# Optimization experiments

Hardware: AMD Instinct MI355X
Metric: run time of the kernel (lower is better)

The kernel has to match this reference:

```python
import jax, jax.numpy as jnp
import numpy as np

B, T, C = 4, 2048, 768
NH = 12
HD = C // NH  # 64


def setup_inputs() -> dict:
    key = jax.random.key(0)
    k1, k2, k3 = jax.random.split(key, 3)
    x = jax.random.normal(k1, (B, T, C), dtype=jnp.float32)
    W_attn = jax.random.normal(k2, (C, 3 * C), dtype=jnp.float32) * (1.0 / np.sqrt(C))
    b_attn = jnp.zeros((3 * C,), dtype=jnp.float32)
    W_proj = jax.random.normal(k3, (C, C), dtype=jnp.float32) * (1.0 / np.sqrt(C))
    b_proj = jnp.zeros((C,), dtype=jnp.float32)
    return {"x": x, "W_attn": W_attn, "b_attn": b_attn, "W_proj": W_proj, "b_proj": b_proj}


def reference(x, W_attn, b_attn, W_proj, b_proj):
    b, t, c = x.shape
    nh, hd = NH, c // NH
    qkv = x @ W_attn + b_attn                      # (B,T,3C)
    q, k, v = jnp.split(qkv, 3, axis=2)
    # (B,T,C) -> (B,NH,T,HD)
    q = q.reshape(b, t, nh, hd).transpose(0, 2, 1, 3)
    k = k.reshape(b, t, nh, hd).transpose(0, 2, 1, 3)
    v = v.reshape(b, t, nh, hd).transpose(0, 2, 1, 3)
    att = jnp.einsum('bhqd,bhkd->bhqk', q, k) / jnp.sqrt(jnp.float32(hd))
    causal = jnp.tril(jnp.ones((t, t), dtype=bool))
    att = jnp.where(causal, att, -jnp.inf)
    att = jax.nn.softmax(att, axis=-1)
    y = jnp.einsum('bhqk,bhkd->bhqd', att, v)      # (B,NH,T,HD)
    y = y.transpose(0, 2, 1, 3).reshape(b, t, c)
    return y @ W_proj + b_proj
```

## Files before the change

### kernel.cpp

```cpp
#include <hip/hip_runtime.h>
#include <hip/hip_bf16.h>
#include <cstdint>

typedef __bf16 bf16;
typedef __bf16 bf16x4 __attribute__((ext_vector_type(4)));
typedef __bf16 bf16x8 __attribute__((ext_vector_type(8)));
typedef float f32x4 __attribute__((ext_vector_type(4)));

#define B_  4
#define T_  2048
#define C_  768
#define NH_ 12
#define HD_ 64
#define BH_ (B_ * NH_)

__device__ __forceinline__ f32x4 mfma16(bf16x8 a, bf16x8 b, f32x4 c) {
  return __builtin_amdgcn_mfma_f32_16x16x32_bf16(a, b, c, 0, 0, 0);
}

__device__ __forceinline__ void gload16(const bf16* src, bf16* dst) {
  __builtin_amdgcn_global_load_lds(
      (const __attribute__((address_space(1))) unsigned int*)src,
      (__attribute__((address_space(3))) unsigned int*)dst, 16, 0, 0);
}

__global__ __launch_bounds__(256) void cvt_kernel(const float* __restrict__ in,
                                                  bf16* __restrict__ out, int n4) {
  int i = blockIdx.x * blockDim.x + threadIdx.x;
  if (i < n4) {
    float4 v = reinterpret_cast<const float4*>(in)[i];
    bf16x4 o;
    o[0] = (bf16)v.x; o[1] = (bf16)v.y; o[2] = (bf16)v.z; o[3] = (bf16)v.w;
    reinterpret_cast<bf16x4*>(out)[i] = o;
  }
}

__global__ __launch_bounds__(256) void wtr_kernel(const float* __restrict__ W,
                                                  bf16* __restrict__ WT, int K, int N) {
  __shared__ bf16 t[64][72];
  const int tid = threadIdx.x;
  const int k0 = blockIdx.x * 64, n0 = blockIdx.y * 64;
  {
    const int r = tid >> 2, cg = (tid & 3) * 16;
    const float* src = W + (size_t)(k0 + r) * N + n0 + cg;
    float4 a0 = reinterpret_cast<const float4*>(src)[0];
    float4 a1 = reinterpret_cast<const float4*>(src)[1];
    float4 a2 = reinterpret_cast<const float4*>(src)[2];
    float4 a3 = reinterpret_cast<const float4*>(src)[3];
    bf16x8 lo, hi;
    lo[0]=(bf16)a0.x; lo[1]=(bf16)a0.y; lo[2]=(bf16)a0.z; lo[3]=(bf16)a0.w;
    lo[4]=(bf16)a1.x; lo[5]=(bf16)a1.y; lo[6]=(bf16)a1.z; lo[7]=(bf16)a1.w;
    hi[0]=(bf16)a2.x; hi[1]=(bf16)a2.y; hi[2]=(bf16)a2.z; hi[3]=(bf16)a2.w;
    hi[4]=(bf16)a3.x; hi[5]=(bf16)a3.y; hi[6]=(bf16)a3.z; hi[7]=(bf16)a3.w;
    *reinterpret_cast<bf16x8*>(&t[r][cg]) = lo;
    *reinterpret_cast<bf16x8*>(&t[r][cg + 8]) = hi;
  }
  __syncthreads();
  {
    const int n = tid & 63, kg = (tid >> 6) * 16;
    bf16x8 o0, o1;
#pragma unroll
    for (int i = 0; i < 8; ++i) { o0[i] = t[kg + i][n]; o1[i] = t[kg + 8 + i][n]; }
    bf16* dst = WT + (size_t)(n0 + n) * K + k0 + kg;
    *reinterpret_cast<bf16x8*>(dst) = o0;
    *reinterpret_cast<bf16x8*>(dst + 8) = o1;
  }
}

template <int EPI>
__global__ __launch_bounds__(256) void gemm_mfma(
    const bf16* __restrict__ A, const bf16* __restrict__ BT,
    const float* __restrict__ bias, int M, int N, int K,
    bf16* __restrict__ q, bf16* __restrict__ k_, bf16* __restrict__ v,
    float* __restrict__ out) {
  __shared__ bf16 AlF[128 * 32];
  __shared__ bf16 BlF[128 * 32];

  const int tid = threadIdx.x;
  const int wid = tid >> 6, lane = tid & 63;
  const int m0 = blockIdx.y * 128, n0 = blockIdx.x * 128;
  const int wm = (wid >> 1) * 64, wn = (wid & 1) * 64;
  const int r = lane & 15, g = lane >> 4;

  f32x4 acc[4][4] = {};

  const int srow = tid >> 2;
  const int scol = (tid & 3) * 8;

  for (int k0 = 0; k0 < K; k0 += 32) {
    __syncthreads();
#pragma unroll
    for (int c = 0; c < 2; ++c) {
      gload16(A  + (size_t)(m0 + c * 64 + srow) * K + k0 + scol, AlF + c * 2048 + wid * 512);
      gload16(BT + (size_t)(n0 + c * 64 + srow) * K + k0 + scol, BlF + c * 2048 + wid * 512);
    }
    __syncthreads();

    bf16x8 af[4], bfr[4];
#pragma unroll
    for (int fm = 0; fm < 4; ++fm)
      af[fm] = *reinterpret_cast<bf16x8*>(&AlF[(wm + fm * 16 + r) * 32 + g * 8]);
#pragma unroll
    for (int fn = 0; fn < 4; ++fn)
      bfr[fn] = *reinterpret_cast<bf16x8*>(&BlF[(wn + fn * 16 + r) * 32 + g * 8]);
#pragma unroll
    for (int fm = 0; fm < 4; ++fm)
#pragma unroll
      for (int fn = 0; fn < 4; ++fn)
        acc[fm][fn] = mfma16(af[fm], bfr[fn], acc[fm][fn]);
  }

#pragma unroll
  for (int fm = 0; fm < 4; ++fm)
#pragma unroll
    for (int fn = 0; fn < 4; ++fn)
#pragma unroll
      for (int j = 0; j < 4; ++j) {
        int m = m0 + wm + fm * 16 + g * 4 + j;
        int n = n0 + wn + fn * 16 + r;
        float val = acc[fm][fn][j] + bias[n];
        if (EPI == 0) {
          int b = m >> 11, t = m & 2047;
          bf16* dst; int c;
          if (n < 768)        { dst = q;  c = n;        val *= 0.125f; }
          else if (n < 1536)  { dst = k_; c = n - 768;  }
          else                { dst = v;  c = n - 1536; }
          int h = c >> 6, d = c & 63;
          dst[(((size_t)(b * NH_ + h)) * T_ + t) * HD_ + d] = (bf16)val;
        } else {
          out[(size_t)m * N + n] = val;
        }
      }
}

__global__ __launch_bounds__(256) void attn_fwd(
    const bf16* __restrict__ Q, const bf16* __restrict__ K,
    const bf16* __restrict__ V, bf16* __restrict__ Y) {
  __shared__ bf16 Kl[64][72];
  __shared__ bf16 VtF[64 * 72];
  __shared__ bf16 Pl[4][16][72];

  const int tid = threadIdx.x;
  const int wid = tid >> 6, lane = tid & 63;
  const int r = lane & 15, g = lane >> 4;
  const int bh = blockIdx.y;
  const int bidx = bh / NH_, h = bh % NH_;

  const bf16* Qb = Q + (size_t)bh * T_ * HD_;
  const bf16* Kb = K + (size_t)bh * T_ * HD_;
  const bf16* Vb = V + (size_t)bh * T_ * HD_;

  const int krow = tid >> 3;
  const int kc8 = (tid & 7) * 8;

#pragma unroll
  for (int pass = 0; pass < 2; ++pass) {
    const int tile = pass ? 31 - blockIdx.x : blockIdx.x;
    const int qt0 = tile * 64 + wid * 16;

    bf16x8 qf[2];
#pragma unroll
    for (int kc = 0; kc < 2; ++kc)
      qf[kc] = *reinterpret_cast<const bf16x8*>(
          Qb + (size_t)(qt0 + r) * HD_ + kc * 32 + g * 8);

    float m_st[4], l_st[4];
    f32x4 o[4] = {};
#pragma unroll
    for (int j = 0; j < 4; ++j) { m_st[j] = -INFINITY; l_st[j] = 0.f; }

    const int nsteps = tile + 1;
    for (int s = 0; s < nsteps; ++s) {
      const int kv0 = s * 64;
      __syncthreads();
#pragma unroll
      for (int p = 0; p < 2; ++p) {
        int row = p * 32 + krow;
        bf16x8 kv8 = *reinterpret_cast<const bf16x8*>(Kb + (size_t)(kv0 + row) * HD_ + kc8);
        *reinterpret_cast<bf16x8*>(&Kl[row][kc8]) = kv8;
        bf16x8 vv8 = *reinterpret_cast<const bf16x8*>(Vb + (size_t)(kv0 + row) * HD_ + kc8);
        int xorb = (((row >> 3) ^ (tid & 7)) << 3) + (row & 7);
#pragma unroll
        for (int j = 0; j < 8; ++j) VtF[(kc8 + j) * 72 + xorb] = vv8[j];
      }
      __syncthreads();

      f32x4 s4[4] = {};
      __builtin_amdgcn_s_setprio(1);
#pragma unroll
      for (int cb = 0; cb < 4; ++cb)
#pragma unroll
        for (int kc = 0; kc < 2; ++kc) {
          bf16x8 kf = *reinterpret_cast<bf16x8*>(&Kl[cb * 16 + r][kc * 32 + g * 8]);
          s4[cb] = mfma16(qf[kc], kf, s4[cb]);
        }
      __builtin_amdgcn_s_setprio(0);

      if (kv0 + 63 > qt0) {
#pragma unroll
        for (int cb = 0; cb < 4; ++cb)
#pragma unroll
          for (int j = 0; j < 4; ++j) {
            int qr = qt0 + g * 4 + j;
            int kc_ = kv0 + cb * 16 + r;
            if (kc_ > qr) s4[cb][j] = -INFINITY;
          }
      }

      float p[4][4];
#pragma unroll
      for (int j = 0; j < 4; ++j) {
        float mm = fmaxf(fmaxf(s4[0][j], s4[1][j]), fmaxf(s4[2][j], s4[3][j]));
#pragma unroll
        for (int msk = 1; msk < 16; msk <<= 1) mm = fmaxf(mm, __shfl_xor(mm, msk));
        float mn = fmaxf(m_st[j], mm);
        float sc = __expf(m_st[j] - mn);
        float sum = 0.f;
#pragma unroll
        for (int cb = 0; cb < 4; ++cb) {
          float pv = __expf(s4[cb][j] - mn);
          p[cb][j] = pv;
          sum += pv;
        }
#pragma unroll
        for (int msk = 1; msk < 16; msk <<= 1) sum += __shfl_xor(sum, msk);
        l_st[j] = l_st[j] * sc + sum;
        m_st[j] = mn;
#pragma unroll
        for (int dn = 0; dn < 4; ++dn) o[dn][j] *= sc;
      }

#pragma unroll
      for (int cb = 0; cb < 4; ++cb)
#pragma unroll
        for (int j = 0; j < 4; ++j)
          Pl[wid][g * 4 + j][cb * 16 + r] = (bf16)p[cb][j];

      __builtin_amdgcn_s_setprio(1);
#pragma unroll
      for (int kc = 0; kc < 2; ++kc) {
        bf16x8 pf = *reinterpret_cast<bf16x8*>(&Pl[wid][r][kc * 32 + g * 8]);
#pragma unroll
        for (int dn = 0; dn < 4; ++dn) {
          int d = dn * 16 + r;
          bf16x8 vf = *reinterpret_cast<bf16x8*>(
              &VtF[d * 72 + (((4 * kc + g) ^ (d >> 3)) << 3)]);
          o[dn] = mfma16(pf, vf, o[dn]);
        }
      }
      __builtin_amdgcn_s_setprio(0);
    }

#pragma unroll
    for (int j = 0; j < 4; ++j) {
      float inv = 1.f / l_st[j];
      int qrow = qt0 + g * 4 + j;
#pragma unroll
      for (int dn = 0; dn < 4; ++dn) {
        int d = dn * 16 + r;
        Y[((size_t)bidx * T_ + qrow) * C_ + h * HD_ + d] = (bf16)(o[dn][j] * inv);
      }
    }
  }
}

extern "C" void kernel_launch(void* const* d_in, const int* in_sizes, int n_in,
                              void* d_out, int out_size, void* d_ws, size_t ws_size,
                              hipStream_t stream) {
  const float* x  = (const float*)d_in[0];
  const float* Wa = (const float*)d_in[1];
  const float* ba = (const float*)d_in[2];
  const float* Wp = (const float*)d_in[3];
  const float* bp = (const float*)d_in[4];
  float* out = (float*)d_out;

  char* ws = (char*)d_ws;
  size_t off = 0;
  auto alloc = [&](size_t bytes) {
    char* p = ws + off;
    off += (bytes + 255) & ~(size_t)255;
    return p;
  };
  bf16* xb   = (bf16*)alloc((size_t)B_ * T_ * C_ * 2);
  bf16* WaT  = (bf16*)alloc((size_t)C_ * 3 * C_ * 2);
  bf16* WpT  = (bf16*)alloc((size_t)C_ * C_ * 2);
  bf16* Qb   = (bf16*)alloc((size_t)BH_ * T_ * HD_ * 2);
  bf16* Kb   = (bf16*)alloc((size_t)BH_ * T_ * HD_ * 2);
  bf16* Vb   = (bf16*)alloc((size_t)BH_ * T_ * HD_ * 2);
  bf16* Yb   = (bf16*)alloc((size_t)B_ * T_ * C_ * 2);

  const int M = B_ * T_;

  cvt_kernel<<<(M * C_ / 4) / 256, 256, 0, stream>>>(x, xb, M * C_ / 4);
  wtr_kernel<<<dim3(C_ / 64, 3 * C_ / 64), 256, 0, stream>>>(Wa, WaT, C_, 3 * C_);
  wtr_kernel<<<dim3(C_ / 64, C_ / 64), 256, 0, stream>>>(Wp, WpT, C_, C_);

  gemm_mfma<0><<<dim3(3 * C_ / 128, M / 128), 256, 0, stream>>>(
      xb, WaT, ba, M, 3 * C_, C_, Qb, Kb, Vb, nullptr);

  attn_fwd<<<dim3(16, BH_), 256, 0, stream>>>(Qb, Kb, Vb, Yb);

  gemm_mfma<1><<<dim3(C_ / 128, M / 128), 256, 0, stream>>>(
      Yb, WpT, bp, M, C_, C_, nullptr, nullptr, nullptr, out);
}
```

Baseline: 276.6 us.

## Transpose QK^T MFMA, use exp2 with lazy rescale, and swizzle block order

Swaps the MFMA operands for S so that each lane holds the scores of a single query row. The row max and sum then need fewer cross-lane shuffles, and P can be written to LDS as packed bf16x4. The 1/sqrt(d) scale is folded together with log2(e) into Q so that exp2f can be used. The running max is rescaled only when some lane's new max exceeds the old one by more than 8, which skips most rescale passes at the cost of slightly larger intermediate exponent values. Both the GEMM and attention blocks are also remapped to group consecutive work items for XCD/L2 locality.

```diff
diff --git a/kernel.cpp b/kernel.cpp
--- a/kernel.cpp
+++ b/kernel.cpp
@@ -78,7 +78,10 @@
 
   const int tid = threadIdx.x;
   const int wid = tid >> 6, lane = tid & 63;
-  const int m0 = blockIdx.y * 128, n0 = blockIdx.x * 128;
+  unsigned orig = blockIdx.y * gridDim.x + blockIdx.x;
+  unsigned cpx = (gridDim.x * gridDim.y) >> 3;
+  unsigned work = (orig & 7) * cpx + (orig >> 3);
+  const int m0 = (work / gridDim.x) * 128, n0 = (work % gridDim.x) * 128;
   const int wm = (wid >> 1) * 64, wn = (wid & 1) * 64;
   const int r = lane & 15, g = lane >> 4;
 
@@ -122,7 +125,7 @@
         if (EPI == 0) {
           int b = m >> 11, t = m & 2047;
           bf16* dst; int c;
-          if (n < 768)        { dst = q;  c = n;        val *= 0.125f; }
+          if (n < 768)        { dst = q;  c = n;        val *= 0.180336881f; }
           else if (n < 1536)  { dst = k_; c = n - 768;  }
           else                { dst = v;  c = n - 1536; }
           int h = c >> 6, d = c & 63;
@@ -143,7 +146,11 @@
   const int tid = threadIdx.x;
   const int wid = tid >> 6, lane = tid & 63;
   const int r = lane & 15, g = lane >> 4;
-  const int bh = blockIdx.y;
+
+  unsigned orig = blockIdx.y * 16 + blockIdx.x;
+  unsigned work = (orig & 7) * 96 + (orig >> 3);
+  const int bx = work & 15;
+  const int bh = work >> 4;
   const int bidx = bh / NH_, h = bh % NH_;
 
   const bf16* Qb = Q + (size_t)bh * T_ * HD_;
@@ -155,7 +162,7 @@
 
 #pragma unroll
   for (int pass = 0; pass < 2; ++pass) {
-    const int tile = pass ? 31 - blockIdx.x : blockIdx.x;
+    const int tile = pass ? 31 - bx : bx;
     const int qt0 = tile * 64 + wid * 16;
 
     bf16x8 qf[2];
@@ -164,10 +171,9 @@
       qf[kc] = *reinterpret_cast<const bf16x8*>(
           Qb + (size_t)(qt0 + r) * HD_ + kc * 32 + g * 8);
 
-    float m_st[4], l_st[4];
+    float m_st = -INFINITY;
+    float l_p = 0.f;
     f32x4 o[4] = {};
-#pragma unroll
-    for (int j = 0; j < 4; ++j) { m_st[j] = -INFINITY; l_st[j] = 0.f; }
 
     const int nsteps = tile + 1;
     for (int s = 0; s < nsteps; ++s) {
@@ -192,49 +198,53 @@
 #pragma unroll
         for (int kc = 0; kc < 2; ++kc) {
           bf16x8 kf = *reinterpret_cast<bf16x8*>(&Kl[cb * 16 + r][kc * 32 + g * 8]);
-          s4[cb] = mfma16(qf[kc], kf, s4[cb]);
+          s4[cb] = mfma16(kf, qf[kc], s4[cb]);
         }
       __builtin_amdgcn_s_setprio(0);
 
-      if (kv0 + 63 > qt0) {
+      if (s == tile) {
 #pragma unroll
         for (int cb = 0; cb < 4; ++cb)
 #pragma unroll
-          for (int j = 0; j < 4; ++j) {
-            int qr = qt0 + g * 4 + j;
-            int kc_ = kv0 + cb * 16 + r;
-            if (kc_ > qr) s4[cb][j] = -INFINITY;
-          }
-      }
-
-      float p[4][4];
-#pragma unroll
-      for (int j = 0; j < 4; ++j) {
-        float mm = fmaxf(fmaxf(s4[0][j], s4[1][j]), fmaxf(s4[2][j], s4[3][j]));
-#pragma unroll
-        for (int msk = 1; msk < 16; msk <<= 1) mm = fmaxf(mm, __shfl_xor(mm, msk));
-        float mn = fmaxf(m_st[j], mm);
-        float sc = __expf(m_st[j] - mn);
-        float sum = 0.f;
-#pragma unroll
-        for (int cb = 0; cb < 4; ++cb) {
-          float pv = __expf(s4[cb][j] - mn);
-          p[cb][j] = pv;
+          for (int j = 0; j < 4; ++j)
+            if (kv0 + cb * 16 + g * 4 + j > qt0 + r) s4[cb][j] = -INFINITY;
+      }
+
+      float pmax = fmaxf(
+          fmaxf(fmaxf(fmaxf(s4[0][0], s4[0][1]), fmaxf(s4[0][2], s4[0][3])),
+                fmaxf(fmaxf(s4[1][0], s4[1][1]), fmaxf(s4[1][2], s4[1][3]))),
+          fmaxf(fmaxf(fmaxf(s4[2][0], s4[2][1]), fmaxf(s4[2][2], s4[2][3])),
+                fmaxf(fmaxf(s4[3][0], s4[3][1]), fmaxf(s4[3][2], s4[3][3]))));
+      pmax = fmaxf(pmax, __shfl_xor(pmax, 16));
+      pmax = fmaxf(pmax, __shfl_xor(pmax, 32));
+
+      if (!__all(pmax - m_st <= 8.0f)) {
+        float sc = exp2f(m_st - pmax);
+        m_st = pmax;
+        l_p *= sc;
+        float sc0 = __shfl(sc, g * 4 + 0);
+        float sc1 = __shfl(sc, g * 4 + 1);
+        float sc2 = __shfl(sc, g * 4 + 2);
+        float sc3 = __shfl(sc, g * 4 + 3);
+#pragma unroll
+        for (int dn = 0; dn < 4; ++dn) {
+          o[dn][0] *= sc0; o[dn][1] *= sc1; o[dn][2] *= sc2; o[dn][3] *= sc3;
+        }
+      }
+
+      float sum = 0.f;
+#pragma unroll
+      for (int cb = 0; cb < 4; ++cb) {
+        bf16x4 pw;
+#pragma unroll
+        for (int j = 0; j < 4; ++j) {
+          float pv = exp2f(s4[cb][j] - m_st);
           sum += pv;
-        }
-#pragma unroll
-        for (int msk = 1; msk < 16; msk <<= 1) sum += __shfl_xor(sum, msk);
-        l_st[j] = l_st[j] * sc + sum;
-        m_st[j] = mn;
-#pragma unroll
-        for (int dn = 0; dn < 4; ++dn) o[dn][j] *= sc;
-      }
-
-#pragma unroll
-      for (int cb = 0; cb < 4; ++cb)
-#pragma unroll
-        for (int j = 0; j < 4; ++j)
-          Pl[wid][g * 4 + j][cb * 16 + r] = (bf16)p[cb][j];
+          pw[j] = (bf16)pv;
+        }
+        *reinterpret_cast<bf16x4*>(&Pl[wid][r][cb * 16 + g * 4]) = pw;
+      }
+      l_p += sum;
 
       __builtin_amdgcn_s_setprio(1);
 #pragma unroll
@@ -251,9 +261,17 @@
       __builtin_amdgcn_s_setprio(0);
     }
 
+    l_p += __shfl_xor(l_p, 16);
+    l_p += __shfl_xor(l_p, 32);
+    float linv = 1.f / l_p;
+    float i0 = __shfl(linv, g * 4 + 0);
+    float i1 = __shfl(linv, g * 4 + 1);
+    float i2 = __shfl(linv, g * 4 + 2);
+    float i3 = __shfl(linv, g * 4 + 3);
+
 #pragma unroll
     for (int j = 0; j < 4; ++j) {
-      float inv = 1.f / l_st[j];
+      float inv = j == 0 ? i0 : (j == 1 ? i1 : (j == 2 ? i2 : i3));
       int qrow = qt0 + g * 4 + j;
 #pragma unroll
       for (int dn = 0; dn < 4; ++dn) {
```

New measurement: 244.1 us. 1.13x faster.
